# Kernel optimization log

Hardware: AMD Instinct MI355X
Metric: run time of the kernel (lower is better)

## Reference

```python
import jax, jax.numpy as jnp
import numpy as np

F, H, C = 768, 256, 16  # feature_size, lstm_hidden_size, num_classes
B, T = 256, 128         # sentences per doc, words per sentence


def lstm_scan(x, w_ih, w_hh, b, reverse=False):
    """PyTorch-convention LSTM (gates i,f,g,o). x: [B,T,D] -> (outputs [B,T,H], h_T [B,H])."""
    Hh = w_hh.shape[1]
    gx = jnp.einsum('btd,gd->btg', x, w_ih) + b      # [B,T,4H], biases fused
    gx = jnp.swapaxes(gx, 0, 1)                      # [T,B,4H]
    h0 = jnp.zeros((x.shape[0], Hh), x.dtype)
    def step(carry, g):
        h, c = carry
        g = g + h @ w_hh.T
        i, f, gg, o = jnp.split(g, 4, axis=-1)
        c = jax.nn.sigmoid(f) * c + jax.nn.sigmoid(i) * jnp.tanh(gg)
        h = jax.nn.sigmoid(o) * jnp.tanh(c)
        return (h, c), h
    (hT, _), ys = jax.lax.scan(step, (h0, h0), gx, reverse=reverse)
    return jnp.swapaxes(ys, 0, 1), hT


def setup_inputs() -> dict:
    key = jax.random.key(0)
    ks = jax.random.split(key, 16)
    s = 0.1
    return {
        'x': jax.random.normal(ks[0], (B, T, F), jnp.float32),
        'y': jax.random.randint(ks[1], (B,), 0, C),
        'mask': jnp.ones((B, T), bool),
        # BiLSTM forward / reverse directions
        'w_ih_f': jax.random.normal(ks[2], (4 * H, F)) * s,
        'w_hh_f': jax.random.normal(ks[3], (4 * H, H)) * s,
        'b_f': jax.random.normal(ks[4], (4 * H,)) * s,
        'w_ih_r': jax.random.normal(ks[5], (4 * H, F)) * s,
        'w_hh_r': jax.random.normal(ks[6], (4 * H, H)) * s,
        'b_r': jax.random.normal(ks[7], (4 * H,)) * s,
        # word_to_sent LSTM (512 -> 512)
        'w_ih_s': jax.random.normal(ks[8], (8 * H, 2 * H)) * s,
        'w_hh_s': jax.random.normal(ks[9], (8 * H, 2 * H)) * s,
        'b_s': jax.random.normal(ks[10], (8 * H,)) * s,
        # linear + CRF params
        'lin_w': jax.random.normal(ks[11], (C, 2 * H)) * s,
        'lin_b': jnp.zeros((C,)),
        'crf_start': jax.random.normal(ks[12], (C,)) * s,
        'crf_end': jax.random.normal(ks[13], (C,)) * s,
        'crf_trans': jax.random.normal(ks[14], (C, C)) * s,
    }


def reference(x, y, mask, w_ih_f, w_hh_f, b_f, w_ih_r, w_hh_r, b_r,
              w_ih_s, w_hh_s, b_s, lin_w, lin_b, crf_start, crf_end, crf_trans):
    # dropout is identity (eval-mode reference)
    out_f, _ = lstm_scan(x, w_ih_f, w_hh_f, b_f, reverse=False)
    out_r, _ = lstm_scan(x, w_ih_r, w_hh_r, b_r, reverse=True)
    h = jnp.concatenate([out_f, out_r], axis=-1)          # [B,T,2H]
    _, hT = lstm_scan(h, w_ih_s, w_hh_s, b_s)             # [B,2H] final hidden per sentence
    emissions = hT @ lin_w.T + lin_b                      # [B,C] -> CRF sequence of length B

    S = emissions.shape[0]
    # numerator: score of gold tag sequence
    num = (crf_start[y[0]] + emissions[jnp.arange(S), y].sum()
           + crf_trans[y[:-1], y[1:]].sum() + crf_end[y[-1]])
    # denominator: forward algorithm (log partition)
    def fstep(alpha, e_t):
        return jax.nn.logsumexp(alpha[:, None] + crf_trans + e_t[None, :], axis=0), None
    alpha0 = crf_start + emissions[0]
    alphaT, _ = jax.lax.scan(fstep, alpha0, emissions[1:])
    denom = jax.nn.logsumexp(alphaT + crf_end)
    return num - denom  # log-likelihood (sum reduction, single CRF batch)
```

## Files before the change

### kernel.cpp

```cpp
#include <hip/hip_runtime.h>
#include <hip/hip_bf16.h>
#include <stdint.h>


typedef __bf16 bf16_t;
typedef __bf16 bf16x8 __attribute__((ext_vector_type(8)));
typedef __bf16 bf16x4v __attribute__((ext_vector_type(4)));
typedef float f32x4 __attribute__((ext_vector_type(4)));

#define MFMA_BF16(a, b, c) __builtin_amdgcn_mfma_f32_16x16x32_bf16((a), (b), (c), 0, 0, 0)

__device__ __forceinline__ float sigm_(float x) { return 1.f / (1.f + __expf(-x)); }
__device__ __forceinline__ float tanh_(float x) {
  x = fminf(20.f, fmaxf(-20.f, x));
  float e = __expf(-2.f * x);
  return (1.f - e) / (1.f + e);
}

__device__ __forceinline__ unsigned long long aload8(const unsigned long long* p) {
  return __hip_atomic_load(p, __ATOMIC_RELAXED, __HIP_MEMORY_SCOPE_AGENT);
}
__device__ __forceinline__ void astore8(unsigned long long* p, unsigned long long v) {
  __hip_atomic_store(p, v, __ATOMIC_RELAXED, __HIP_MEMORY_SCOPE_AGENT);
}

template <int NG>
__device__ __forceinline__ void wait_flags(const unsigned* base, unsigned tgt) {
  const int lane = threadIdx.x & 63;
  for (;;) {
    unsigned f = tgt;
    if (lane < NG)
      f = __hip_atomic_load(base + lane * 32, __ATOMIC_RELAXED, __HIP_MEMORY_SCOPE_AGENT);
    if (__all((int)(f >= tgt))) break;
    __builtin_amdgcn_s_sleep(2);
  }
  __asm__ __volatile__("" ::: "memory");
}

union U16 { struct { unsigned long long a, b; } s; bf16x8 v; };
union U8  { bf16x4v v; unsigned long long u; };

__global__ void init_bar(unsigned* flags) {
  int i = blockIdx.x * 256 + threadIdx.x;
  flags[i] = 0u;
}

__global__ void cvt4(const float* __restrict__ in, bf16_t* __restrict__ out, int n4) {
  int i = blockIdx.x * blockDim.x + threadIdx.x;
  int stride = gridDim.x * blockDim.x;
  for (; i < n4; i += stride) {
    float4 v = ((const float4*)in)[i];
    bf16x4v o;
    o.x = (bf16_t)v.x; o.y = (bf16_t)v.y; o.z = (bf16_t)v.z; o.w = (bf16_t)v.w;
    ((bf16x4v*)out)[i] = o;
  }
}

__global__ void __launch_bounds__(256, 2)
gemm_bt(const bf16_t* __restrict__ A, const bf16_t* __restrict__ B,
        bf16_t* __restrict__ C, int M, int N, int K) {
  const int tid = threadIdx.x;
  const int w = tid >> 6, lane = tid & 63, quad = lane >> 4, l15 = lane & 15;
  const int ntiles = N >> 7;
  const int m0 = (blockIdx.x / ntiles) << 7;
  const int n0 = (blockIdx.x % ntiles) << 7;
  const int wm = (w >> 1) << 6, wn = (w & 1) << 6;

  __shared__ bf16_t As[128 * 72];
  __shared__ bf16_t Bs[128 * 72];

  const f32x4 z4 = {0.f, 0.f, 0.f, 0.f};
  f32x4 acc[4][4];
#pragma unroll
  for (int i = 0; i < 4; ++i)
#pragma unroll
    for (int j = 0; j < 4; ++j) acc[i][j] = z4;

  const int nk = K >> 6;
  for (int kt = 0; kt < nk; ++kt) {
    uint4 av[4], bv[4];
#pragma unroll
    for (int i = 0; i < 4; ++i) {
      int cid = tid + i * 256;
      int r = cid >> 3, c = cid & 7;
      av[i] = *(const uint4*)&A[(size_t)(m0 + r) * K + kt * 64 + c * 8];
      bv[i] = *(const uint4*)&B[(size_t)(n0 + r) * K + kt * 64 + c * 8];
    }
    __syncthreads();
#pragma unroll
    for (int i = 0; i < 4; ++i) {
      int cid = tid + i * 256;
      int r = cid >> 3, c = cid & 7;
      *(uint4*)&As[r * 72 + c * 8] = av[i];
      *(uint4*)&Bs[r * 72 + c * 8] = bv[i];
    }
    __syncthreads();
#pragma unroll
    for (int s = 0; s < 2; ++s) {
      bf16x8 af[4], bfr[4];
#pragma unroll
      for (int i = 0; i < 4; ++i)
        af[i] = *(const bf16x8*)&As[(wm + i * 16 + l15) * 72 + s * 32 + quad * 8];
#pragma unroll
      for (int j = 0; j < 4; ++j)
        bfr[j] = *(const bf16x8*)&Bs[(wn + j * 16 + l15) * 72 + s * 32 + quad * 8];
#pragma unroll
      for (int i = 0; i < 4; ++i)
#pragma unroll
        for (int j = 0; j < 4; ++j)
          acc[i][j] = MFMA_BF16(af[i], bfr[j], acc[i][j]);
    }
  }
#pragma unroll
  for (int i = 0; i < 4; ++i)
#pragma unroll
    for (int j = 0; j < 4; ++j)
#pragma unroll
      for (int p = 0; p < 4; ++p) {
        int row = m0 + wm + i * 16 + quad * 4 + p;
        int col = n0 + wn + j * 16 + l15;
        C[(size_t)row * N + col] = (bf16_t)acc[i][j][p];
      }
}

__global__ void __launch_bounds__(256, 1)
lstm_fr(const bf16_t* __restrict__ gx, const bf16_t* __restrict__ whh,
        const float* __restrict__ b_f, const float* __restrict__ b_r,
        bf16_t* __restrict__ h_cat, bf16_t* __restrict__ hb,
        unsigned* __restrict__ flags) {
  const int tid = threadIdx.x;
  const int w = tid >> 6, lane = tid & 63, quad = lane >> 4, l15 = lane & 15;
  const int dir = blockIdx.x >> 6;
  const int bg = (blockIdx.x >> 2) & 15;
  const int hsp = blockIdx.x & 3;
  const int rows0 = bg << 4;
  const int hid0 = hsp << 6;
  unsigned* fgrp = flags + (dir * 16 + bg) * 128;
  unsigned* fmine = fgrp + hsp * 32;

  __shared__ bf16_t Ws[256 * 264];
  __shared__ bf16_t hcb[8 * 16 * 64];
  const bf16_t* Wg = whh + (size_t)dir * 262144;
#pragma unroll
  for (int i = 0; i < 32; ++i) {
    int id = tid + i * 256;
    int r = id >> 5, c = id & 31;
    int g = r >> 6, hh = r & 63;
    *(uint4*)&Ws[r * 264 + c * 8] =
        *(const uint4*)&Wg[(size_t)(g * 256 + hid0 + hh) * 256 + c * 8];
  }
  const float* bias = dir ? b_r : b_f;
  const int hid = hid0 + w * 16 + quad * 4;
  float br[4][4];
#pragma unroll
  for (int g = 0; g < 4; ++g)
#pragma unroll
    for (int p = 0; p < 4; ++p) br[g][p] = bias[g * 256 + hid + p];
  const int brow = rows0 + l15;
  float c4[4] = {0.f, 0.f, 0.f, 0.f};
  const f32x4 z4 = {0.f, 0.f, 0.f, 0.f};
  __syncthreads();

  for (int t = 1; t <= 128; ++t) {
    const int tt = dir ? (128 - t) : (t - 1);
    const size_t gbase = ((size_t)brow * 128 + tt) * 2048 + (size_t)dir * 1024;
    bf16x4v gp[4];
#pragma unroll
    for (int g = 0; g < 4; ++g) gp[g] = *(const bf16x4v*)&gx[gbase + g * 256 + hid];

    f32x4 acc[4];
#pragma unroll
    for (int g = 0; g < 4; ++g) acc[g] = z4;

    if (t >= 2) {
      if (w == 0) wait_flags<4>(fgrp, (unsigned)(t - 1));
      __syncthreads();
      const unsigned long long* hrow = (const unsigned long long*)
          (hb + (((size_t)((t & 1) ^ 1) * 2 + dir) * 256 + brow) * 256);
#pragma unroll
      for (int ks = 0; ks < 8; ++ks) {
        U16 u;
        u.s.a = aload8(hrow + ks * 8 + quad * 2);
        u.s.b = aload8(hrow + ks * 8 + quad * 2 + 1);
#pragma unroll
        for (int g = 0; g < 4; ++g) {
          bf16x8 af = *(const bf16x8*)&Ws[(g * 64 + w * 16 + l15) * 264 + ks * 32 + quad * 8];
          acc[g] = MFMA_BF16(af, u.v, acc[g]);
        }
      }
    }
    bf16x4v hv;
#pragma unroll
    for (int p = 0; p < 4; ++p) {
      float Pi = acc[0][p] + (float)gp[0][p] + br[0][p];
      float Pf = acc[1][p] + (float)gp[1][p] + br[1][p];
      float Pg = acc[2][p] + (float)gp[2][p] + br[2][p];
      float Po = acc[3][p] + (float)gp[3][p] + br[3][p];
      float cc = sigm_(Pf) * c4[p] + sigm_(Pi) * tanh_(Pg);
      c4[p] = cc;
      hv[p] = (bf16_t)(sigm_(Po) * tanh_(cc));
    }
    *(bf16x4v*)&hcb[(((t - 1) & 7) * 16 + l15) * 64 + w * 16 + quad * 4] = hv;

    if (t < 128) {
      U8 cv; cv.v = hv;
      astore8((unsigned long long*)(hb + (((size_t)(t & 1) * 2 + dir) * 256 + brow) * 256 + hid),
              cv.u);
      __syncthreads();
      if (tid == 0)
        __hip_atomic_store(fmine, (unsigned)t, __ATOMIC_RELEASE, __HIP_MEMORY_SCOPE_AGENT);
    } else {
      __syncthreads();
    }

    if ((t & 7) == 0) {
      const int r = tid >> 1, half = tid & 1;
      const int tloc = r >> 4, bl = r & 15;
      const int tp = t - 8 + tloc;
      const int ttd = dir ? (127 - tp) : tp;
      const uint4* src = (const uint4*)&hcb[(tloc * 16 + bl) * 64 + half * 32];
      uint4* dst = (uint4*)&h_cat[((size_t)(rows0 + bl) * 128 + ttd) * 512 +
                                  dir * 256 + hid0 + half * 32];
#pragma unroll
      for (int q = 0; q < 4; ++q) dst[q] = src[q];
    }
  }
}

__global__ void __launch_bounds__(256, 1)
lstm_s(const bf16_t* __restrict__ gs, const bf16_t* __restrict__ wsh,
       const float* __restrict__ b_s, float* __restrict__ hT,
       bf16_t* __restrict__ hb, unsigned* __restrict__ flags) {
  const int tid = threadIdx.x;
  const int w = tid >> 6, lane = tid & 63, quad = lane >> 4, l15 = lane & 15;
  const int bg = blockIdx.x >> 4;
  const int hsp = blockIdx.x & 15;
  const int rows0 = bg << 5;
  const int hid0 = hsp << 5;
  const int nt = w & 1, hb2 = w >> 1;
  unsigned* fgrp = flags + bg * 512;
  unsigned* fmine = fgrp + hsp * 32;

  __shared__ bf16_t Ws[128 * 520];
#pragma unroll
  for (int i = 0; i < 32; ++i) {
    int id = tid + i * 256;
    int r = id >> 6, c = id & 63;
    int g = r >> 5, hh = r & 31;
    *(uint4*)&Ws[r * 520 + c * 8] =
        *(const uint4*)&wsh[(size_t)(g * 512 + hid0 + hh) * 512 + c * 8];
  }
  const int hid = hid0 + hb2 * 16 + quad * 4;
  float br[4][4];
#pragma unroll
  for (int g = 0; g < 4; ++g)
#pragma unroll
    for (int p = 0; p < 4; ++p) br[g][p] = b_s[g * 512 + hid + p];
  const int brow = rows0 + nt * 16 + l15;
  float c4[4] = {0.f, 0.f, 0.f, 0.f};
  const f32x4 z4 = {0.f, 0.f, 0.f, 0.f};
  __syncthreads();

  for (int t = 1; t <= 128; ++t) {
    const size_t gbase = ((size_t)brow * 128 + (t - 1)) * 2048;
    bf16x4v gp[4];
#pragma unroll
    for (int g = 0; g < 4; ++g) gp[g] = *(const bf16x4v*)&gs[gbase + g * 512 + hid];

    f32x4 acc[4];
#pragma unroll
    for (int g = 0; g < 4; ++g) acc[g] = z4;

    if (t >= 2) {
      if (w == 0) wait_flags<16>(fgrp, (unsigned)(t - 1));
      __syncthreads();
      const unsigned long long* hrow = (const unsigned long long*)
          (hb + ((size_t)((t & 1) ^ 1) * 256 + brow) * 512);
#pragma unroll
      for (int ks = 0; ks < 16; ++ks) {
        U16 u;
        u.s.a = aload8(hrow + ks * 8 + quad * 2);
        u.s.b = aload8(hrow + ks * 8 + quad * 2 + 1);
#pragma unroll
        for (int g = 0; g < 4; ++g) {
          bf16x8 af = *(const bf16x8*)&Ws[(g * 32 + hb2 * 16 + l15) * 520 + ks * 32 + quad * 8];
          acc[g] = MFMA_BF16(af, u.v, acc[g]);
        }
      }
    }
    bf16x4v hv;
    float hf[4];
#pragma unroll
    for (int p = 0; p < 4; ++p) {
      float Pi = acc[0][p] + (float)gp[0][p] + br[0][p];
      float Pf = acc[1][p] + (float)gp[1][p] + br[1][p];
      float Pg = acc[2][p] + (float)gp[2][p] + br[2][p];
      float Po = acc[3][p] + (float)gp[3][p] + br[3][p];
      float cc = sigm_(Pf) * c4[p] + sigm_(Pi) * tanh_(Pg);
      c4[p] = cc;
      hf[p] = sigm_(Po) * tanh_(cc);
      hv[p] = (bf16_t)hf[p];
    }
    if (t < 128) {
      U8 cv; cv.v = hv;
      astore8((unsigned long long*)(hb + ((size_t)(t & 1) * 256 + brow) * 512 + hid), cv.u);
      __syncthreads();
      if (tid == 0)
        __hip_atomic_store(fmine, (unsigned)t, __ATOMIC_RELEASE, __HIP_MEMORY_SCOPE_AGENT);
    } else {
      *(float4*)&hT[(size_t)brow * 512 + hid] = make_float4(hf[0], hf[1], hf[2], hf[3]);
    }
  }
}

__global__ void emis_k(const float* __restrict__ hT, const float* __restrict__ lin_w,
                       const float* __restrict__ lin_b, float* __restrict__ em) {
  const int idx = blockIdx.x * 256 + threadIdx.x;
  const int s = idx >> 4, c = idx & 15;
  const float4* h4 = (const float4*)(hT + (size_t)s * 512);
  const float4* w4 = (const float4*)(lin_w + (size_t)c * 512);
  float acc = lin_b[c];
  for (int k = 0; k < 128; ++k) {
    float4 a = h4[k], b = w4[k];
    acc += a.x * b.x + a.y * b.y + a.z * b.z + a.w * b.w;
  }
  em[idx] = acc;
}

__global__ void crf_k(const float* __restrict__ em, const int* __restrict__ y,
                      const float* __restrict__ cs, const float* __restrict__ ce,
                      const float* __restrict__ tr, float* __restrict__ out) {
  __shared__ float alpha[16];
  __shared__ float trs[256];
  const int lane = threadIdx.x;
  const int i = lane & 15, jg = lane >> 4;

  for (int k = lane; k < 256; k += 64) trs[k] = tr[k];
  __syncthreads();

  float np = 0.f;
  for (int s = lane; s < 256; s += 64) np += em[s * 16 + y[s]];
  for (int s = lane + 1; s < 256; s += 64) np += trs[y[s - 1] * 16 + y[s]];
#pragma unroll
  for (int off = 32; off > 0; off >>= 1) np += __shfl_down(np, off, 64);

  if (lane < 16) alpha[lane] = cs[lane] + em[lane];
  __syncthreads();

  for (int s = 1; s < 256; ++s) {
    const float* e = em + s * 16;
    float v[4];
#pragma unroll
    for (int jj = 0; jj < 4; ++jj) v[jj] = alpha[i] + trs[i * 16 + (jj * 4 + jg)];
    float res[4];
#pragma unroll
    for (int jj = 0; jj < 4; ++jj) {
      float m = v[jj];
      m = fmaxf(m, __shfl_xor(m, 1, 64));
      m = fmaxf(m, __shfl_xor(m, 2, 64));
      m = fmaxf(m, __shfl_xor(m, 4, 64));
      m = fmaxf(m, __shfl_xor(m, 8, 64));
      float ex = __expf(v[jj] - m);
      ex += __shfl_xor(ex, 1, 64);
      ex += __shfl_xor(ex, 2, 64);
      ex += __shfl_xor(ex, 4, 64);
      ex += __shfl_xor(ex, 8, 64);
      res[jj] = m + __logf(ex) + e[jj * 4 + jg];
    }
#pragma unroll
    for (int jj = 0; jj < 4; ++jj)
      if (i == 0) alpha[jj * 4 + jg] = res[jj];
  }

  float v = (lane < 16) ? (alpha[lane] + ce[lane]) : -3.0e38f;
  float m = v;
#pragma unroll
  for (int off = 32; off > 0; off >>= 1) m = fmaxf(m, __shfl_xor(m, off, 64));
  float ex = __expf(v - m);
#pragma unroll
  for (int off = 32; off > 0; off >>= 1) ex += __shfl_xor(ex, off, 64);
  float denom = m + __logf(ex);

  if (lane == 0) {
    float num = np + cs[y[0]] + ce[y[255]];
    out[0] = num - denom;
  }
}

extern "C" void kernel_launch(void* const* d_in, const int* in_sizes, int n_in,
                              void* d_out, int out_size, void* d_ws, size_t ws_size,
                              hipStream_t stream) {
  const float* x = (const float*)d_in[0];
  const int* y = (const int*)d_in[1];
  const float* w_ih_f = (const float*)d_in[3];
  const float* w_hh_f = (const float*)d_in[4];
  const float* b_f = (const float*)d_in[5];
  const float* w_ih_r = (const float*)d_in[6];
  const float* w_hh_r = (const float*)d_in[7];
  const float* b_r = (const float*)d_in[8];
  const float* w_ih_s = (const float*)d_in[9];
  const float* w_hh_s = (const float*)d_in[10];
  const float* b_s = (const float*)d_in[11];
  const float* lin_w = (const float*)d_in[12];
  const float* lin_b = (const float*)d_in[13];
  const float* crf_s = (const float*)d_in[14];
  const float* crf_e = (const float*)d_in[15];
  const float* crf_t = (const float*)d_in[16];

  char* ws = (char*)d_ws;
  size_t off = 0;
  auto take = [&](size_t bytes) {
    void* p = ws + off;
    off += (bytes + 255) & ~(size_t)255;
    return p;
  };
  bf16_t* Wx  = (bf16_t*)take((size_t)2048 * 768 * 2);
  bf16_t* Whh = (bf16_t*)take((size_t)2 * 1024 * 256 * 2);
  bf16_t* Wsi = (bf16_t*)take((size_t)2048 * 512 * 2);
  bf16_t* Wsh = (bf16_t*)take((size_t)2048 * 512 * 2);
  bf16_t* gx  = (bf16_t*)take((size_t)32768 * 2048 * 2);
  bf16_t* xb  = (bf16_t*)take((size_t)32768 * 768 * 2);
  float* hT   = (float*)take((size_t)256 * 512 * 4);
  float* em   = (float*)take((size_t)4096 * 4);
  bf16_t* gs = gx;
  bf16_t* hcat = xb;
  char* tail = (char*)xb + 33554432;
  bf16_t* hb_fr = (bf16_t*)tail;
  bf16_t* hb_s  = (bf16_t*)(tail + 524288);
  unsigned* flags_fr = (unsigned*)(tail + 1048576);
  unsigned* flags_s  = (unsigned*)(tail + 1048576 + 16384);
  (void)ws_size; (void)in_sizes; (void)n_in; (void)out_size;

  cvt4<<<2048, 256, 0, stream>>>(x, xb, 32768 * 768 / 4);
  cvt4<<<64, 256, 0, stream>>>(w_ih_f, Wx, 786432 / 4);
  cvt4<<<64, 256, 0, stream>>>(w_ih_r, Wx + 786432, 786432 / 4);
  cvt4<<<32, 256, 0, stream>>>(w_hh_f, Whh, 262144 / 4);
  cvt4<<<32, 256, 0, stream>>>(w_hh_r, Whh + 262144, 262144 / 4);
  cvt4<<<64, 256, 0, stream>>>(w_ih_s, Wsi, 1048576 / 4);
  cvt4<<<64, 256, 0, stream>>>(w_hh_s, Wsh, 1048576 / 4);

  gemm_bt<<<4096, 256, 0, stream>>>(xb, Wx, gx, 32768, 2048, 768);

  init_bar<<<32, 256, 0, stream>>>(flags_fr);

  lstm_fr<<<128, 256, 0, stream>>>(gx, Whh, b_f, b_r, hcat, hb_fr, flags_fr);

  gemm_bt<<<4096, 256, 0, stream>>>(hcat, Wsi, gs, 32768, 2048, 512);

  lstm_s<<<128, 256, 0, stream>>>(gs, Wsh, b_s, hT, hb_s, flags_s);

  emis_k<<<16, 256, 0, stream>>>(hT, lin_w, lin_b, em);
  crf_k<<<1, 64, 0, stream>>>(em, y, crf_s, crf_e, crf_t, (float*)d_out);
}
```

Measured before the change: 3.130 ms.

## Replace flag barriers with step-tagged hidden-state words in recurrent LSTM kernels

The cross-block flag barrier plus __syncthreads per timestep is replaced by a protocol where each 64-bit hidden-state word carries the timestep in its upper half. Consumers poll the data directly and issue the loads before the gate-input loads, and a 4-deep ring buffer prevents overwrite races. This removes the flag round trip and block-wide barriers from the serial recurrence critical path. It also writes h_cat directly instead of staging through shared memory, at the cost of doubled hb traffic and spin loops on per-chunk data.

New measurement: 4.113 ms. +31.4%, slower.

```diff
diff --git a/kernel.cpp b/kernel.cpp
--- a/kernel.cpp
+++ b/kernel.cpp
@@ -7,6 +7,7 @@
 typedef __bf16 bf16x8 __attribute__((ext_vector_type(8)));
 typedef __bf16 bf16x4v __attribute__((ext_vector_type(4)));
 typedef float f32x4 __attribute__((ext_vector_type(4)));
+typedef unsigned long long u64;
 
 #define MFMA_BF16(a, b, c) __builtin_amdgcn_mfma_f32_16x16x32_bf16((a), (b), (c), 0, 0, 0)
 
@@ -17,32 +18,20 @@
   return (1.f - e) / (1.f + e);
 }
 
-__device__ __forceinline__ unsigned long long aload8(const unsigned long long* p) {
+__device__ __forceinline__ u64 aload8(const u64* p) {
   return __hip_atomic_load(p, __ATOMIC_RELAXED, __HIP_MEMORY_SCOPE_AGENT);
 }
-__device__ __forceinline__ void astore8(unsigned long long* p, unsigned long long v) {
+__device__ __forceinline__ void astore8(u64* p, u64 v) {
   __hip_atomic_store(p, v, __ATOMIC_RELAXED, __HIP_MEMORY_SCOPE_AGENT);
 }
 
-template <int NG>
-__device__ __forceinline__ void wait_flags(const unsigned* base, unsigned tgt) {
-  const int lane = threadIdx.x & 63;
-  for (;;) {
-    unsigned f = tgt;
-    if (lane < NG)
-      f = __hip_atomic_load(base + lane * 32, __ATOMIC_RELAXED, __HIP_MEMORY_SCOPE_AGENT);
-    if (__all((int)(f >= tgt))) break;
-    __builtin_amdgcn_s_sleep(2);
-  }
-  __asm__ __volatile__("" ::: "memory");
-}
-
-union U16 { struct { unsigned long long a, b; } s; bf16x8 v; };
-union U8  { bf16x4v v; unsigned long long u; };
-
-__global__ void init_bar(unsigned* flags) {
+union U8 { bf16x4v v; uint2 u; };
+union B8 { uint32_t u[4]; bf16x8 v; };
+
+__global__ void zero8(u64* __restrict__ p, int n) {
   int i = blockIdx.x * 256 + threadIdx.x;
-  flags[i] = 0u;
+  int s = gridDim.x * 256;
+  for (; i < n; i += s) p[i] = 0ull;
 }
 
 __global__ void cvt4(const float* __restrict__ in, bf16_t* __restrict__ out, int n4) {
@@ -126,8 +115,7 @@
 __global__ void __launch_bounds__(256, 1)
 lstm_fr(const bf16_t* __restrict__ gx, const bf16_t* __restrict__ whh,
         const float* __restrict__ b_f, const float* __restrict__ b_r,
-        bf16_t* __restrict__ h_cat, bf16_t* __restrict__ hb,
-        unsigned* __restrict__ flags) {
+        bf16_t* __restrict__ h_cat, u64* __restrict__ hb) {
   const int tid = threadIdx.x;
   const int w = tid >> 6, lane = tid & 63, quad = lane >> 4, l15 = lane & 15;
   const int dir = blockIdx.x >> 6;
@@ -135,11 +123,8 @@
   const int hsp = blockIdx.x & 3;
   const int rows0 = bg << 4;
   const int hid0 = hsp << 6;
-  unsigned* fgrp = flags + (dir * 16 + bg) * 128;
-  unsigned* fmine = fgrp + hsp * 32;
 
   __shared__ bf16_t Ws[256 * 264];
-  __shared__ bf16_t hcb[8 * 16 * 64];
   const bf16_t* Wg = whh + (size_t)dir * 262144;
 #pragma unroll
   for (int i = 0; i < 32; ++i) {
@@ -163,6 +148,16 @@
 
   for (int t = 1; t <= 128; ++t) {
     const int tt = dir ? (128 - t) : (t - 1);
+
+    u64 wv[8][4];
+    if (t >= 2) {
+      const u64* hrow = hb + (((size_t)((t - 1) & 3) * 2 + dir) * 256 + brow) * 128;
+#pragma unroll
+      for (int ks = 0; ks < 8; ++ks)
+#pragma unroll
+        for (int p = 0; p < 4; ++p)
+          wv[ks][p] = aload8(hrow + ks * 16 + quad * 4 + p);
+    }
     const size_t gbase = ((size_t)brow * 128 + tt) * 2048 + (size_t)dir * 1024;
     bf16x4v gp[4];
 #pragma unroll
@@ -173,19 +168,36 @@
     for (int g = 0; g < 4; ++g) acc[g] = z4;
 
     if (t >= 2) {
-      if (w == 0) wait_flags<4>(fgrp, (unsigned)(t - 1));
-      __syncthreads();
-      const unsigned long long* hrow = (const unsigned long long*)
-          (hb + (((size_t)((t & 1) ^ 1) * 2 + dir) * 256 + brow) * 256);
+      const u64* hrow = hb + (((size_t)((t - 1) & 3) * 2 + dir) * 256 + brow) * 128;
+      const unsigned expt = (unsigned)(t - 1);
+      unsigned ready = 0;
+      while (ready != 0xFFu) {
+#pragma unroll
+        for (int ks = 0; ks < 8; ++ks)
+          if (!(ready & (1u << ks))) {
+            bool ok = ((unsigned)(wv[ks][0] >> 32) == expt) &&
+                      ((unsigned)(wv[ks][1] >> 32) == expt) &&
+                      ((unsigned)(wv[ks][2] >> 32) == expt) &&
+                      ((unsigned)(wv[ks][3] >> 32) == expt);
+            if (__all((int)ok)) {
+              ready |= 1u << ks;
+            } else {
+#pragma unroll
+              for (int p = 0; p < 4; ++p)
+                wv[ks][p] = aload8(hrow + ks * 16 + quad * 4 + p);
+            }
+          }
+        __asm__ __volatile__("" ::: "memory");
+      }
 #pragma unroll
       for (int ks = 0; ks < 8; ++ks) {
-        U16 u;
-        u.s.a = aload8(hrow + ks * 8 + quad * 2);
-        u.s.b = aload8(hrow + ks * 8 + quad * 2 + 1);
+        B8 Bv;
+#pragma unroll
+        for (int p = 0; p < 4; ++p) Bv.u[p] = (uint32_t)wv[ks][p];
 #pragma unroll
         for (int g = 0; g < 4; ++g) {
           bf16x8 af = *(const bf16x8*)&Ws[(g * 64 + w * 16 + l15) * 264 + ks * 32 + quad * 8];
-          acc[g] = MFMA_BF16(af, u.v, acc[g]);
+          acc[g] = MFMA_BF16(af, Bv.v, acc[g]);
         }
       }
     }
@@ -200,29 +212,14 @@
       c4[p] = cc;
       hv[p] = (bf16_t)(sigm_(Po) * tanh_(cc));
     }
-    *(bf16x4v*)&hcb[(((t - 1) & 7) * 16 + l15) * 64 + w * 16 + quad * 4] = hv;
+    *(bf16x4v*)&h_cat[((size_t)brow * 128 + tt) * 512 + dir * 256 + hid] = hv;
 
     if (t < 128) {
       U8 cv; cv.v = hv;
-      astore8((unsigned long long*)(hb + (((size_t)(t & 1) * 2 + dir) * 256 + brow) * 256 + hid),
-              cv.u);
-      __syncthreads();
-      if (tid == 0)
-        __hip_atomic_store(fmine, (unsigned)t, __ATOMIC_RELEASE, __HIP_MEMORY_SCOPE_AGENT);
-    } else {
-      __syncthreads();
-    }
-
-    if ((t & 7) == 0) {
-      const int r = tid >> 1, half = tid & 1;
-      const int tloc = r >> 4, bl = r & 15;
-      const int tp = t - 8 + tloc;
-      const int ttd = dir ? (127 - tp) : tp;
-      const uint4* src = (const uint4*)&hcb[(tloc * 16 + bl) * 64 + half * 32];
-      uint4* dst = (uint4*)&h_cat[((size_t)(rows0 + bl) * 128 + ttd) * 512 +
-                                  dir * 256 + hid0 + half * 32];
-#pragma unroll
-      for (int q = 0; q < 4; ++q) dst[q] = src[q];
+      const u64 tag = (u64)(unsigned)t << 32;
+      u64* orow = hb + (((size_t)(t & 3) * 2 + dir) * 256 + brow) * 128 + (hid >> 1);
+      astore8(orow,     (u64)cv.u.x | tag);
+      astore8(orow + 1, (u64)cv.u.y | tag);
     }
   }
 }
@@ -230,7 +227,7 @@
 __global__ void __launch_bounds__(256, 1)
 lstm_s(const bf16_t* __restrict__ gs, const bf16_t* __restrict__ wsh,
        const float* __restrict__ b_s, float* __restrict__ hT,
-       bf16_t* __restrict__ hb, unsigned* __restrict__ flags) {
+       u64* __restrict__ hb) {
   const int tid = threadIdx.x;
   const int w = tid >> 6, lane = tid & 63, quad = lane >> 4, l15 = lane & 15;
   const int bg = blockIdx.x >> 4;
@@ -238,8 +235,6 @@
   const int rows0 = bg << 5;
   const int hid0 = hsp << 5;
   const int nt = w & 1, hb2 = w >> 1;
-  unsigned* fgrp = flags + bg * 512;
-  unsigned* fmine = fgrp + hsp * 32;
 
   __shared__ bf16_t Ws[128 * 520];
 #pragma unroll
@@ -262,6 +257,15 @@
   __syncthreads();
 
   for (int t = 1; t <= 128; ++t) {
+    u64 wv[16][4];
+    if (t >= 2) {
+      const u64* hrow = hb + ((size_t)((t - 1) & 3) * 256 + brow) * 256;
+#pragma unroll
+      for (int ks = 0; ks < 16; ++ks)
+#pragma unroll
+        for (int p = 0; p < 4; ++p)
+          wv[ks][p] = aload8(hrow + ks * 16 + quad * 4 + p);
+    }
     const size_t gbase = ((size_t)brow * 128 + (t - 1)) * 2048;
     bf16x4v gp[4];
 #pragma unroll
@@ -272,19 +276,36 @@
     for (int g = 0; g < 4; ++g) acc[g] = z4;
 
     if (t >= 2) {
-      if (w == 0) wait_flags<16>(fgrp, (unsigned)(t - 1));
-      __syncthreads();
-      const unsigned long long* hrow = (const unsigned long long*)
-          (hb + ((size_t)((t & 1) ^ 1) * 256 + brow) * 512);
+      const u64* hrow = hb + ((size_t)((t - 1) & 3) * 256 + brow) * 256;
+      const unsigned expt = (unsigned)(t - 1);
+      unsigned ready = 0;
+      while (ready != 0xFFFFu) {
+#pragma unroll
+        for (int ks = 0; ks < 16; ++ks)
+          if (!(ready & (1u << ks))) {
+            bool ok = ((unsigned)(wv[ks][0] >> 32) == expt) &&
+                      ((unsigned)(wv[ks][1] >> 32) == expt) &&
+                      ((unsigned)(wv[ks][2] >> 32) == expt) &&
+                      ((unsigned)(wv[ks][3] >> 32) == expt);
+            if (__all((int)ok)) {
+              ready |= 1u << ks;
+            } else {
+#pragma unroll
+              for (int p = 0; p < 4; ++p)
+                wv[ks][p] = aload8(hrow + ks * 16 + quad * 4 + p);
+            }
+          }
+        __asm__ __volatile__("" ::: "memory");
+      }
 #pragma unroll
       for (int ks = 0; ks < 16; ++ks) {
-        U16 u;
-        u.s.a = aload8(hrow + ks * 8 + quad * 2);
-        u.s.b = aload8(hrow + ks * 8 + quad * 2 + 1);
+        B8 Bv;
+#pragma unroll
+        for (int p = 0; p < 4; ++p) Bv.u[p] = (uint32_t)wv[ks][p];
 #pragma unroll
         for (int g = 0; g < 4; ++g) {
           bf16x8 af = *(const bf16x8*)&Ws[(g * 32 + hb2 * 16 + l15) * 520 + ks * 32 + quad * 8];
-          acc[g] = MFMA_BF16(af, u.v, acc[g]);
+          acc[g] = MFMA_BF16(af, Bv.v, acc[g]);
         }
       }
     }
@@ -303,10 +324,10 @@
     }
     if (t < 128) {
       U8 cv; cv.v = hv;
-      astore8((unsigned long long*)(hb + ((size_t)(t & 1) * 256 + brow) * 512 + hid), cv.u);
-      __syncthreads();
-      if (tid == 0)
-        __hip_atomic_store(fmine, (unsigned)t, __ATOMIC_RELEASE, __HIP_MEMORY_SCOPE_AGENT);
+      const u64 tag = (u64)(unsigned)t << 32;
+      u64* orow = hb + ((size_t)(t & 3) * 256 + brow) * 256 + (hid >> 1);
+      astore8(orow,     (u64)cv.u.x | tag);
+      astore8(orow + 1, (u64)cv.u.y | tag);
     } else {
       *(float4*)&hT[(size_t)brow * 512 + hid] = make_float4(hf[0], hf[1], hf[2], hf[3]);
     }
@@ -425,10 +446,8 @@
   bf16_t* gs = gx;
   bf16_t* hcat = xb;
   char* tail = (char*)xb + 33554432;
-  bf16_t* hb_fr = (bf16_t*)tail;
-  bf16_t* hb_s  = (bf16_t*)(tail + 524288);
-  unsigned* flags_fr = (unsigned*)(tail + 1048576);
-  unsigned* flags_s  = (unsigned*)(tail + 1048576 + 16384);
+  u64* hb_fr = (u64*)tail;
+  u64* hb_s  = (u64*)(tail + 2097152);
   (void)ws_size; (void)in_sizes; (void)n_in; (void)out_size;
 
   cvt4<<<2048, 256, 0, stream>>>(x, xb, 32768 * 768 / 4);
@@ -441,13 +460,13 @@
 
   gemm_bt<<<4096, 256, 0, stream>>>(xb, Wx, gx, 32768, 2048, 768);
 
-  init_bar<<<32, 256, 0, stream>>>(flags_fr);
-
-  lstm_fr<<<128, 256, 0, stream>>>(gx, Whh, b_f, b_r, hcat, hb_fr, flags_fr);
+  zero8<<<512, 256, 0, stream>>>(hb_fr, 524288);
+
+  lstm_fr<<<128, 256, 0, stream>>>(gx, Whh, b_f, b_r, hcat, hb_fr);
 
   gemm_bt<<<4096, 256, 0, stream>>>(hcat, Wsi, gs, 32768, 2048, 512);
 
-  lstm_s<<<128, 256, 0, stream>>>(gs, Wsh, b_s, hT, hb_s, flags_s);
+  lstm_s<<<128, 256, 0, stream>>>(gs, Wsh, b_s, hT, hb_s);
 
   emis_k<<<16, 256, 0, stream>>>(hT, lin_w, lin_b, em);
   crf_k<<<1, 64, 0, stream>>>(em, y, crf_s, crf_e, crf_t, (float*)d_out);
```

## Replace block barriers with per-wave flags in recurrent LSTM kernels

Applied to the files above, without the earlier changes.

Each wave now publishes its own progress flag and polls the group's flags directly, so the per-step __syncthreads barriers are gone. Flags are packed contiguously, one per wave, and the block-to-group mapping is interleaved. The LDS staging buffer for h_cat is dropped; each wave writes its hidden state straight to global memory every step. This targets barrier and synchronisation latency on the serial critical path, at the cost of smaller scattered global stores and more polling traffic.

After: 4.750 ms. +51.8%, slower.

```diff
diff --git a/kernel.cpp b/kernel.cpp
--- a/kernel.cpp
+++ b/kernel.cpp
@@ -7,6 +7,7 @@
 typedef __bf16 bf16x8 __attribute__((ext_vector_type(8)));
 typedef __bf16 bf16x4v __attribute__((ext_vector_type(4)));
 typedef float f32x4 __attribute__((ext_vector_type(4)));
+typedef unsigned long long u64;
 
 #define MFMA_BF16(a, b, c) __builtin_amdgcn_mfma_f32_16x16x32_bf16((a), (b), (c), 0, 0, 0)
 
@@ -17,32 +18,20 @@
   return (1.f - e) / (1.f + e);
 }
 
-__device__ __forceinline__ unsigned long long aload8(const unsigned long long* p) {
+__device__ __forceinline__ u64 aload8(const u64* p) {
   return __hip_atomic_load(p, __ATOMIC_RELAXED, __HIP_MEMORY_SCOPE_AGENT);
 }
-__device__ __forceinline__ void astore8(unsigned long long* p, unsigned long long v) {
+__device__ __forceinline__ void astore8(u64* p, u64 v) {
   __hip_atomic_store(p, v, __ATOMIC_RELAXED, __HIP_MEMORY_SCOPE_AGENT);
-}
-
-template <int NG>
-__device__ __forceinline__ void wait_flags(const unsigned* base, unsigned tgt) {
-  const int lane = threadIdx.x & 63;
-  for (;;) {
-    unsigned f = tgt;
-    if (lane < NG)
-      f = __hip_atomic_load(base + lane * 32, __ATOMIC_RELAXED, __HIP_MEMORY_SCOPE_AGENT);
-    if (__all((int)(f >= tgt))) break;
-    __builtin_amdgcn_s_sleep(2);
-  }
-  __asm__ __volatile__("" ::: "memory");
 }
 
 union U16 { struct { unsigned long long a, b; } s; bf16x8 v; };
 union U8  { bf16x4v v; unsigned long long u; };
 
-__global__ void init_bar(unsigned* flags) {
+__global__ void zero8(u64* __restrict__ p, int n) {
   int i = blockIdx.x * 256 + threadIdx.x;
-  flags[i] = 0u;
+  int s = gridDim.x * 256;
+  for (; i < n; i += s) p[i] = 0ull;
 }
 
 __global__ void cvt4(const float* __restrict__ in, bf16_t* __restrict__ out, int n4) {
@@ -130,16 +119,16 @@
         unsigned* __restrict__ flags) {
   const int tid = threadIdx.x;
   const int w = tid >> 6, lane = tid & 63, quad = lane >> 4, l15 = lane & 15;
-  const int dir = blockIdx.x >> 6;
-  const int bg = (blockIdx.x >> 2) & 15;
-  const int hsp = blockIdx.x & 3;
+  const int grp = blockIdx.x & 31;
+  const int hsp = blockIdx.x >> 5;
+  const int dir = grp >> 4;
+  const int bg = grp & 15;
   const int rows0 = bg << 4;
   const int hid0 = hsp << 6;
-  unsigned* fgrp = flags + (dir * 16 + bg) * 128;
-  unsigned* fmine = fgrp + hsp * 32;
+  unsigned* fgrp = flags + grp * 32;
+  unsigned* fmine = fgrp + (hsp * 4 + w);
 
   __shared__ bf16_t Ws[256 * 264];
-  __shared__ bf16_t hcb[8 * 16 * 64];
   const bf16_t* Wg = whh + (size_t)dir * 262144;
 #pragma unroll
   for (int i = 0; i < 32; ++i) {
@@ -173,9 +162,16 @@
     for (int g = 0; g < 4; ++g) acc[g] = z4;
 
     if (t >= 2) {
-      if (w == 0) wait_flags<4>(fgrp, (unsigned)(t - 1));
-      __syncthreads();
-      const unsigned long long* hrow = (const unsigned long long*)
+      const unsigned tgt = (unsigned)(t - 1);
+      for (;;) {
+        unsigned f = tgt;
+        if (lane < 16)
+          f = __hip_atomic_load(fgrp + lane, __ATOMIC_RELAXED, __HIP_MEMORY_SCOPE_AGENT);
+        if (__all((int)(f >= tgt))) break;
+        __builtin_amdgcn_s_sleep(2);
+      }
+      __asm__ __volatile__("" ::: "memory");
+      const u64* hrow = (const u64*)
           (hb + (((size_t)((t & 1) ^ 1) * 2 + dir) * 256 + brow) * 256);
 #pragma unroll
       for (int ks = 0; ks < 8; ++ks) {
@@ -200,30 +196,13 @@
       c4[p] = cc;
       hv[p] = (bf16_t)(sigm_(Po) * tanh_(cc));
     }
-    *(bf16x4v*)&hcb[(((t - 1) & 7) * 16 + l15) * 64 + w * 16 + quad * 4] = hv;
-
     if (t < 128) {
       U8 cv; cv.v = hv;
-      astore8((unsigned long long*)(hb + (((size_t)(t & 1) * 2 + dir) * 256 + brow) * 256 + hid),
-              cv.u);
-      __syncthreads();
-      if (tid == 0)
+      astore8((u64*)(hb + (((size_t)(t & 1) * 2 + dir) * 256 + brow) * 256 + hid), cv.u);
+      if (lane == 0)
         __hip_atomic_store(fmine, (unsigned)t, __ATOMIC_RELEASE, __HIP_MEMORY_SCOPE_AGENT);
-    } else {
-      __syncthreads();
-    }
-
-    if ((t & 7) == 0) {
-      const int r = tid >> 1, half = tid & 1;
-      const int tloc = r >> 4, bl = r & 15;
-      const int tp = t - 8 + tloc;
-      const int ttd = dir ? (127 - tp) : tp;
-      const uint4* src = (const uint4*)&hcb[(tloc * 16 + bl) * 64 + half * 32];
-      uint4* dst = (uint4*)&h_cat[((size_t)(rows0 + bl) * 128 + ttd) * 512 +
-                                  dir * 256 + hid0 + half * 32];
-#pragma unroll
-      for (int q = 0; q < 4; ++q) dst[q] = src[q];
-    }
+    }
+    *(bf16x4v*)&h_cat[((size_t)brow * 128 + tt) * 512 + dir * 256 + hid] = hv;
   }
 }
 
@@ -233,13 +212,14 @@
        bf16_t* __restrict__ hb, unsigned* __restrict__ flags) {
   const int tid = threadIdx.x;
   const int w = tid >> 6, lane = tid & 63, quad = lane >> 4, l15 = lane & 15;
-  const int bg = blockIdx.x >> 4;
-  const int hsp = blockIdx.x & 15;
+  const int bg = blockIdx.x & 7;
+  const int hsp = blockIdx.x >> 3;
   const int rows0 = bg << 5;
   const int hid0 = hsp << 5;
   const int nt = w & 1, hb2 = w >> 1;
-  unsigned* fgrp = flags + bg * 512;
-  unsigned* fmine = fgrp + hsp * 32;
+  unsigned* fgrp = flags + bg * 64;
+  unsigned* fmine = fgrp + (hsp * 4 + w);
+  const int pline = ((lane >> 1) << 2) | ((lane & 1) << 1) | nt;
 
   __shared__ bf16_t Ws[128 * 520];
 #pragma unroll
@@ -272,9 +252,16 @@
     for (int g = 0; g < 4; ++g) acc[g] = z4;
 
     if (t >= 2) {
-      if (w == 0) wait_flags<16>(fgrp, (unsigned)(t - 1));
-      __syncthreads();
-      const unsigned long long* hrow = (const unsigned long long*)
+      const unsigned tgt = (unsigned)(t - 1);
+      for (;;) {
+        unsigned f = tgt;
+        if (lane < 32)
+          f = __hip_atomic_load(fgrp + pline, __ATOMIC_RELAXED, __HIP_MEMORY_SCOPE_AGENT);
+        if (__all((int)(f >= tgt))) break;
+        __builtin_amdgcn_s_sleep(2);
+      }
+      __asm__ __volatile__("" ::: "memory");
+      const u64* hrow = (const u64*)
           (hb + ((size_t)((t & 1) ^ 1) * 256 + brow) * 512);
 #pragma unroll
       for (int ks = 0; ks < 16; ++ks) {
@@ -303,9 +290,8 @@
     }
     if (t < 128) {
       U8 cv; cv.v = hv;
-      astore8((unsigned long long*)(hb + ((size_t)(t & 1) * 256 + brow) * 512 + hid), cv.u);
-      __syncthreads();
-      if (tid == 0)
+      astore8((u64*)(hb + ((size_t)(t & 1) * 256 + brow) * 512 + hid), cv.u);
+      if (lane == 0)
         __hip_atomic_store(fmine, (unsigned)t, __ATOMIC_RELEASE, __HIP_MEMORY_SCOPE_AGENT);
     } else {
       *(float4*)&hT[(size_t)brow * 512 + hid] = make_float4(hf[0], hf[1], hf[2], hf[3]);
@@ -428,7 +414,7 @@
   bf16_t* hb_fr = (bf16_t*)tail;
   bf16_t* hb_s  = (bf16_t*)(tail + 524288);
   unsigned* flags_fr = (unsigned*)(tail + 1048576);
-  unsigned* flags_s  = (unsigned*)(tail + 1048576 + 16384);
+  unsigned* flags_s  = flags_fr + 1024;
   (void)ws_size; (void)in_sizes; (void)n_in; (void)out_size;
 
   cvt4<<<2048, 256, 0, stream>>>(x, xb, 32768 * 768 / 4);
@@ -441,7 +427,7 @@
 
   gemm_bt<<<4096, 256, 0, stream>>>(xb, Wx, gx, 32768, 2048, 768);
 
-  init_bar<<<32, 256, 0, stream>>>(flags_fr);
+  zero8<<<8, 256, 0, stream>>>((u64*)flags_fr, 768);
 
   lstm_fr<<<128, 256, 0, stream>>>(gx, Whh, b_f, b_r, hcat, hb_fr, flags_fr);
 
```
